# Performance work log

Hardware: AMD Instinct MI355X
Metric: run time of the kernel (lower is better)

Reference implementation:

```python
import jax, jax.numpy as jnp
import numpy as np

NUM_HEADS = 16
HIDDEN = 1024
HEAD = HIDDEN // NUM_HEADS


def setup_inputs() -> dict:
    key = jax.random.key(0)
    k1, k2, k3, k4, k5 = jax.random.split(key, 5)
    b, s, d = 2, 2048, HIDDEN
    scale = 1.0 / np.sqrt(d)
    return {
        "features": jax.random.normal(k1, (b, s, d), dtype=jnp.float32),
        "qkv_w": jax.random.normal(k2, (3 * d, d), dtype=jnp.float32) * scale,  # torch Linear weight [out,in]
        "qkv_b": jax.random.normal(k3, (3 * d,), dtype=jnp.float32) * 0.01,
        "out_w": jax.random.normal(k4, (d, d), dtype=jnp.float32) * scale,
        "out_b": jax.random.normal(k5, (d,), dtype=jnp.float32) * 0.01,
        "use_causal_mask": 0,
    }


def reference(features, qkv_w, qkv_b, out_w, out_b, use_causal_mask):
    b, s, d = features.shape
    qkv = features @ qkv_w.T + qkv_b                      # [b,s,3d]
    q, k, v = jnp.split(qkv, 3, axis=-1)
    # [b,s,d] -> [b,h,s,hd]
    def heads(x):
        return x.reshape(b, s, NUM_HEADS, HEAD).transpose(0, 2, 1, 3)
    q, k, v = heads(q), heads(k), heads(v)
    scores = jnp.einsum("bhqd,bhkd->bhqk", q, k) / np.sqrt(HEAD)
    if use_causal_mask:
        mask = jnp.triu(jnp.ones((s, s), dtype=bool), k=1)
        scores = jnp.where(mask, -jnp.inf, scores)
    attn = jax.nn.softmax(scores, axis=-1)
    out = jnp.einsum("bhqk,bhkd->bhqd", attn, v)          # [b,h,s,hd]
    out = out.transpose(0, 2, 1, 3).reshape(b, s, d)
    return out @ out_w.T + out_b
```

## Files before the change

kernel.cpp:

```cpp
#include <hip/hip_runtime.h>
#include <math.h>

#define BATCH 2
#define SEQ   2048
#define HID   1024
#define NHEAD 16
#define ROWS  (BATCH*SEQ)
#define QKV_N (3*HID)

#define Q_SCALE 0.18033688011112042f

typedef __attribute__((ext_vector_type(8))) short bf16x8;
typedef __attribute__((ext_vector_type(4))) float f32x4;

__device__ __forceinline__ unsigned short f2b(float f) {
    unsigned u = __float_as_uint(f);
    u += 0x7FFF + ((u >> 16) & 1);
    return (unsigned short)(u >> 16);
}
__device__ __forceinline__ unsigned pk2(float a, float b) {
    return (unsigned)f2b(a) | ((unsigned)f2b(b) << 16);
}

#define GLOAD_LDS16(gp, lp) \
    __builtin_amdgcn_global_load_lds((const __attribute__((address_space(1))) void*)(gp), \
                                     (__attribute__((address_space(3))) void*)(lp), 16, 0, 0)

__global__ __launch_bounds__(256)
void cvt_all(const float* __restrict__ a, unsigned short* __restrict__ oa, int na4,
             const float* __restrict__ b, unsigned short* __restrict__ ob, int nb4,
             const float* __restrict__ c, unsigned short* __restrict__ oc, int nc4) {
    int i = blockIdx.x * 256 + threadIdx.x;
    const float* src; unsigned short* dst; int j;
    if (i < na4)            { src = a; dst = oa; j = i; }
    else if (i < na4 + nb4) { src = b; dst = ob; j = i - na4; }
    else if (i < na4 + nb4 + nc4) { src = c; dst = oc; j = i - na4 - nb4; }
    else return;
    float4 v = reinterpret_cast<const float4*>(src)[j];
    ushort4 o;
    o.x = f2b(v.x); o.y = f2b(v.y); o.z = f2b(v.z); o.w = f2b(v.w);
    reinterpret_cast<ushort4*>(dst)[j] = o;
}

template<int MODE>
__global__ __launch_bounds__(256)
void gemm_mfma(const unsigned short* __restrict__ A, const unsigned short* __restrict__ B,
               const float* __restrict__ bias, void* __restrict__ Cout,
               unsigned short* __restrict__ vt, int M, int N, int K) {
    __shared__ __align__(16) unsigned short As[128 * 32];
    __shared__ __align__(16) unsigned short Bs[128 * 32];
    const int tid = threadIdx.x;
    const int w = tid >> 6, l = tid & 63;
    const int wm = w >> 1, wn = w & 1;
    const int l15 = l & 15, l4 = l >> 4;
    const long row0 = (long)blockIdx.y * 128;
    const long col0 = (long)blockIdx.x * 128;

    f32x4 acc[4][4];
    #pragma unroll
    for (int m = 0; m < 4; ++m)
        #pragma unroll
        for (int n = 0; n < 4; ++n) acc[m][n] = (f32x4)0.0f;

    const int lr   = l >> 2;
    const int slot = (l & 3) ^ (lr & 3);

    for (int k0 = 0; k0 < K; k0 += 32) {
        __syncthreads();
        #pragma unroll
        for (int c = 0; c < 2; ++c) {
            int r = w * 32 + c * 16 + lr;
            GLOAD_LDS16(A + (row0 + r) * K + k0 + slot * 8, As + (w * 32 + c * 16) * 32);
            GLOAD_LDS16(B + (col0 + r) * K + k0 + slot * 8, Bs + (w * 32 + c * 16) * 32);
        }
        __syncthreads();

        bf16x8 af[4], bfr[4];
        #pragma unroll
        for (int m = 0; m < 4; ++m) {
            int row = wm * 64 + m * 16 + l15;
            af[m] = *(const bf16x8*)((const char*)As + row * 64 + ((l4 ^ (row & 3)) << 4));
        }
        #pragma unroll
        for (int n = 0; n < 4; ++n) {
            int row = wn * 64 + n * 16 + l15;
            bfr[n] = *(const bf16x8*)((const char*)Bs + row * 64 + ((l4 ^ (row & 3)) << 4));
        }
        #pragma unroll
        for (int m = 0; m < 4; ++m)
            #pragma unroll
            for (int n = 0; n < 4; ++n)
                acc[m][n] = __builtin_amdgcn_mfma_f32_16x16x32_bf16(af[m], bfr[n], acc[m][n], 0, 0, 0);
    }

    #pragma unroll
    for (int m = 0; m < 4; ++m) {
        #pragma unroll
        for (int n = 0; n < 4; ++n) {
            long ccol = col0 + wn * 64 + n * 16 + l15;
            float bv = bias[ccol];
            #pragma unroll
            for (int r2 = 0; r2 < 4; ++r2) {
                long crow = row0 + wm * 64 + m * 16 + l4 * 4 + r2;
                float v = acc[m][n][r2] + bv;
                if (MODE == 0) {
                    ((float*)Cout)[crow * N + ccol] = v;
                } else {
                    if (ccol < 1024) {
                        ((unsigned short*)Cout)[crow * QKV_N + ccol] = f2b(v * Q_SCALE);
                    } else if (ccol < 2048) {
                        ((unsigned short*)Cout)[crow * QKV_N + ccol] = f2b(v);
                    } else {
                        long cc = ccol - 2048;
                        long h = cc >> 6, d = cc & 63;
                        long b = crow >> 11, s = crow & 2047;
                        vt[(((b * NHEAD + h) * 64 + d) << 11) + s] = f2b(v);
                    }
                }
            }
        }
    }
}

__global__ __launch_bounds__(256)
void attn_mfma(const unsigned short* __restrict__ qkv, const unsigned short* __restrict__ vt,
               unsigned short* __restrict__ attno, const int* __restrict__ use_mask) {
    __shared__ __align__(16) unsigned short Ks [64 * 64];
    __shared__ __align__(16) unsigned short Vts[64 * 64];
    __shared__ __align__(16) unsigned short Ps [4][32 * 64];
    const int tid = threadIdx.x;
    const int w = tid >> 6, l = tid & 63;
    const int l15 = l & 15, l4 = l >> 4;
    const int bid  = blockIdx.x;
    const int orig = (bid & 7) * 64 + (bid >> 3);
    const int qt = orig & 15, bh = orig >> 4;
    const int b = bh >> 4, h = bh & 15;
    const int q0 = qt * 128;
    const int wq0 = q0 + w * 32;
    const int causal = use_mask[0];
    const int NT = causal ? 2 * (qt + 1) : (SEQ / 64);

    bf16x8 qf[2][2];
    #pragma unroll
    for (int m = 0; m < 2; ++m) {
        const unsigned short* qp = qkv + (size_t)(b * SEQ + wq0 + m * 16 + l15) * QKV_N + h * 64;
        qf[m][0] = *(const bf16x8*)(qp + l4 * 8);
        qf[m][1] = *(const bf16x8*)(qp + 32 + l4 * 8);
    }

    f32x4 o_acc[2][4];
    #pragma unroll
    for (int m = 0; m < 2; ++m)
        #pragma unroll
        for (int n = 0; n < 4; ++n) o_acc[m][n] = (f32x4)0.0f;
    f32x4 l_acc[2] = {(f32x4)0.0f, (f32x4)0.0f};

    bf16x8 ones;
    #pragma unroll
    for (int j = 0; j < 8; ++j) ones[j] = (short)0x3F80;

    const int srow = l >> 3, g = l & 7;
    const int r0   = w * 16 + srow;
    const int wso  = (g ^ srow) << 3;
    const unsigned short* kbase = qkv + (size_t)b * SEQ * QKV_N + HID + h * 64;
    const unsigned short* vbase = vt + (size_t)bh * 64 * SEQ;
    unsigned short* pw = Ps[w];

    bf16x8 kreg[2], vreg[2];
    #pragma unroll
    for (int c = 0; c < 2; ++c) {
        kreg[c] = *(const bf16x8*)(kbase + (size_t)(r0 + c * 8) * QKV_N + g * 8);
        vreg[c] = *(const bf16x8*)(vbase + (size_t)(r0 + c * 8) * SEQ + g * 8);
    }

    for (int kt = 0; kt < NT; ++kt) {
        __syncthreads();
        #pragma unroll
        for (int c = 0; c < 2; ++c) {
            *(bf16x8*)(Ks  + (r0 + c * 8) * 64 + wso) = kreg[c];
            *(bf16x8*)(Vts + (r0 + c * 8) * 64 + wso) = vreg[c];
        }
        __syncthreads();

        if (kt + 1 < NT) {
            int nk0 = (kt + 1) * 64;
            #pragma unroll
            for (int c = 0; c < 2; ++c) {
                kreg[c] = *(const bf16x8*)(kbase + (size_t)(nk0 + r0 + c * 8) * QKV_N + g * 8);
                vreg[c] = *(const bf16x8*)(vbase + (size_t)(r0 + c * 8) * SEQ + nk0 + g * 8);
            }
        }

        f32x4 s_acc[4][2];
        #pragma unroll
        for (int n = 0; n < 4; ++n)
            #pragma unroll
            for (int m = 0; m < 2; ++m) s_acc[n][m] = (f32x4)0.0f;
        #pragma unroll
        for (int ks = 0; ks < 2; ++ks) {
            #pragma unroll
            for (int n = 0; n < 4; ++n) {
                int row = n * 16 + l15;
                bf16x8 kf = *(const bf16x8*)((const char*)Ks + row * 128 + (((ks * 4 + l4) ^ (row & 7)) << 4));
                #pragma unroll
                for (int m = 0; m < 2; ++m)
                    s_acc[n][m] = __builtin_amdgcn_mfma_f32_16x16x32_bf16(kf, qf[m][ks], s_acc[n][m], 0, 0, 0);
            }
        }
        if (causal) {
            int kk0 = kt * 64;
            #pragma unroll
            for (int n = 0; n < 4; ++n)
                #pragma unroll
                for (int m = 0; m < 2; ++m)
                    #pragma unroll
                    for (int r2 = 0; r2 < 4; ++r2) {
                        int krow = kk0 + n * 16 + l4 * 4 + r2;
                        int qcol = wq0 + m * 16 + l15;
                        if (krow > qcol) s_acc[n][m][r2] = -INFINITY;
                    }
        }

        #pragma unroll
        for (int m = 0; m < 2; ++m) {
            int prow = m * 16 + l15;
            #pragma unroll
            for (int n = 0; n < 4; ++n) {
                float p0 = exp2f(s_acc[n][m][0]);
                float p1 = exp2f(s_acc[n][m][1]);
                float p2 = exp2f(s_acc[n][m][2]);
                float p3 = exp2f(s_acc[n][m][3]);
                uint2 pk;
                pk.x = pk2(p0, p1);
                pk.y = pk2(p2, p3);
                int byteoff = (n * 32 + l4 * 8) ^ ((prow & 7) << 4);
                *(uint2*)((char*)pw + prow * 128 + byteoff) = pk;
            }
        }

        #pragma unroll
        for (int ks = 0; ks < 2; ++ks) {
            bf16x8 pf[2];
            #pragma unroll
            for (int m = 0; m < 2; ++m) {
                int row = m * 16 + l15;
                pf[m] = *(const bf16x8*)((const char*)pw + row * 128 + (((ks * 4 + l4) ^ (row & 7)) << 4));
                l_acc[m] = __builtin_amdgcn_mfma_f32_16x16x32_bf16(pf[m], ones, l_acc[m], 0, 0, 0);
            }
            #pragma unroll
            for (int n = 0; n < 4; ++n) {
                int vrow = n * 16 + l15;
                bf16x8 vf = *(const bf16x8*)((const char*)Vts + vrow * 128 + (((ks * 4 + l4) ^ (vrow & 7)) << 4));
                #pragma unroll
                for (int m = 0; m < 2; ++m)
                    o_acc[m][n] = __builtin_amdgcn_mfma_f32_16x16x32_bf16(pf[m], vf, o_acc[m][n], 0, 0, 0);
            }
        }
    }

    #pragma unroll
    for (int m = 0; m < 2; ++m) {
        #pragma unroll
        for (int r2 = 0; r2 < 4; ++r2) {
            float inv = 1.0f / l_acc[m][r2];
            size_t orow = (size_t)(b * SEQ + wq0 + m * 16 + l4 * 4 + r2);
            #pragma unroll
            for (int n = 0; n < 4; ++n)
                attno[orow * HID + h * 64 + n * 16 + l15] = f2b(o_acc[m][n][r2] * inv);
        }
    }
}

extern "C" void kernel_launch(void* const* d_in, const int* in_sizes, int n_in,
                              void* d_out, int out_size, void* d_ws, size_t ws_size,
                              hipStream_t stream) {
    const float* features = (const float*)d_in[0];
    const float* qkv_w    = (const float*)d_in[1];
    const float* qkv_b    = (const float*)d_in[2];
    const float* out_w    = (const float*)d_in[3];
    const float* out_b    = (const float*)d_in[4];
    const int*   use_mask = (const int*)d_in[5];

    char* ws = (char*)d_ws;
    unsigned short* fbf     = (unsigned short*)(ws);
    unsigned short* wbf     = (unsigned short*)(ws + 8388608);
    unsigned short* owbf    = (unsigned short*)(ws + 14680064);
    unsigned short* qkvbf   = (unsigned short*)(ws + 16777216);
    unsigned short* vtbuf   = (unsigned short*)(ws + 41943040);
    unsigned short* attnobf = (unsigned short*)(ws + 50331648);

    cvt_all<<<8192, 256, 0, stream>>>(features, fbf, 1048576,
                                      qkv_w, wbf, 786432,
                                      out_w, owbf, 262144);

    dim3 g1(QKV_N / 128, ROWS / 128);
    gemm_mfma<2><<<g1, 256, 0, stream>>>(fbf, wbf, qkv_b, (void*)qkvbf, vtbuf,
                                         ROWS, QKV_N, HID);

    attn_mfma<<<512, 256, 0, stream>>>(qkvbf, vtbuf, attnobf, use_mask);

    dim3 g3(HID / 128, ROWS / 128);
    gemm_mfma<0><<<g3, 256, 0, stream>>>(attnobf, owbf, out_b, d_out, (unsigned short*)nullptr,
                                         ROWS, HID, HID);
}
```

Measured before the change: 156.0 us.

## Split attention key tiles across wave pairs and double grid size

The attention kernel now uses 64-query blocks with 1024 blocks instead of 128-query blocks with 512. Each pair of waves shares a 32-query slice but handles a different 32-key half of every key tile. The partial output and row sums of the two halves are combined through LDS at the end. It also adds s_setprio around the MFMA sections, a packed bf16 conversion intrinsic, occupancy launch bounds and incremental pointer arithmetic. The aim is more parallelism and occupancy on the device, at the cost of loading K/V tiles twice as often per query and an extra reduction step.

```diff
diff --git a/kernel.cpp b/kernel.cpp
--- a/kernel.cpp
+++ b/kernel.cpp
@@ -1,4 +1,5 @@
 #include <hip/hip_runtime.h>
+#include <hip/hip_bf16.h>
 #include <math.h>
 
 #define BATCH 2
@@ -18,8 +19,10 @@
     u += 0x7FFF + ((u >> 16) & 1);
     return (unsigned short)(u >> 16);
 }
-__device__ __forceinline__ unsigned pk2(float a, float b) {
-    return (unsigned)f2b(a) | ((unsigned)f2b(b) << 16);
+__device__ __forceinline__ unsigned pk2c(float a, float b) {
+    __hip_bfloat162 h = __float22bfloat162_rn(float2{a, b});
+    union { __hip_bfloat162 h2; unsigned u; } cv; cv.h2 = h;
+    return cv.u;
 }
 
 #define GLOAD_LDS16(gp, lp) \
@@ -122,23 +125,24 @@
     }
 }
 
-__global__ __launch_bounds__(256)
+__global__ __launch_bounds__(256, 4)
 void attn_mfma(const unsigned short* __restrict__ qkv, const unsigned short* __restrict__ vt,
                unsigned short* __restrict__ attno, const int* __restrict__ use_mask) {
     __shared__ __align__(16) unsigned short Ks [64 * 64];
     __shared__ __align__(16) unsigned short Vts[64 * 64];
-    __shared__ __align__(16) unsigned short Ps [4][32 * 64];
+    __shared__ __align__(16) unsigned short Ps [4][32 * 32];
     const int tid = threadIdx.x;
     const int w = tid >> 6, l = tid & 63;
     const int l15 = l & 15, l4 = l >> 4;
     const int bid  = blockIdx.x;
-    const int orig = (bid & 7) * 64 + (bid >> 3);
-    const int qt = orig & 15, bh = orig >> 4;
+    const int orig = (bid & 7) * 128 + (bid >> 3);
+    const int qt = orig & 31, bh = orig >> 5;
     const int b = bh >> 4, h = bh & 15;
-    const int q0 = qt * 128;
-    const int wq0 = q0 + w * 32;
+    const int q0 = qt * 64;
+    const int qh = w & 1, kh = w >> 1;
+    const int wq0 = q0 + qh * 32;
     const int causal = use_mask[0];
-    const int NT = causal ? 2 * (qt + 1) : (SEQ / 64);
+    const int NT = causal ? (qt + 1) : (SEQ / 64);
 
     bf16x8 qf[2][2];
     #pragma unroll
@@ -162,16 +166,19 @@
     const int srow = l >> 3, g = l & 7;
     const int r0   = w * 16 + srow;
     const int wso  = (g ^ srow) << 3;
-    const unsigned short* kbase = qkv + (size_t)b * SEQ * QKV_N + HID + h * 64;
-    const unsigned short* vbase = vt + (size_t)bh * 64 * SEQ;
     unsigned short* pw = Ps[w];
 
+    const unsigned short* kp = qkv + (size_t)b * SEQ * QKV_N + HID + h * 64
+                                   + (size_t)r0 * QKV_N + g * 8;
+    const unsigned short* vp = vt + (size_t)bh * 64 * SEQ + (size_t)r0 * SEQ + g * 8;
+
     bf16x8 kreg[2], vreg[2];
-    #pragma unroll
-    for (int c = 0; c < 2; ++c) {
-        kreg[c] = *(const bf16x8*)(kbase + (size_t)(r0 + c * 8) * QKV_N + g * 8);
-        vreg[c] = *(const bf16x8*)(vbase + (size_t)(r0 + c * 8) * SEQ + g * 8);
-    }
+    kreg[0] = *(const bf16x8*)(kp);
+    kreg[1] = *(const bf16x8*)(kp + 8 * QKV_N);
+    vreg[0] = *(const bf16x8*)(vp);
+    vreg[1] = *(const bf16x8*)(vp + 8 * SEQ);
+    kp += (size_t)64 * QKV_N;
+    vp += 64;
 
     for (int kt = 0; kt < NT; ++kt) {
         __syncthreads();
@@ -183,41 +190,44 @@
         __syncthreads();
 
         if (kt + 1 < NT) {
-            int nk0 = (kt + 1) * 64;
-            #pragma unroll
-            for (int c = 0; c < 2; ++c) {
-                kreg[c] = *(const bf16x8*)(kbase + (size_t)(nk0 + r0 + c * 8) * QKV_N + g * 8);
-                vreg[c] = *(const bf16x8*)(vbase + (size_t)(r0 + c * 8) * SEQ + nk0 + g * 8);
-            }
-        }
-
-        f32x4 s_acc[4][2];
-        #pragma unroll
-        for (int n = 0; n < 4; ++n)
-            #pragma unroll
-            for (int m = 0; m < 2; ++m) s_acc[n][m] = (f32x4)0.0f;
+            kreg[0] = *(const bf16x8*)(kp);
+            kreg[1] = *(const bf16x8*)(kp + 8 * QKV_N);
+            vreg[0] = *(const bf16x8*)(vp);
+            vreg[1] = *(const bf16x8*)(vp + 8 * SEQ);
+            kp += (size_t)64 * QKV_N;
+            vp += 64;
+        }
+
+        f32x4 s_acc[2][2];
+        #pragma unroll
+        for (int n2 = 0; n2 < 2; ++n2)
+            #pragma unroll
+            for (int m = 0; m < 2; ++m) s_acc[n2][m] = (f32x4)0.0f;
+        __builtin_amdgcn_s_setprio(1);
         #pragma unroll
         for (int ks = 0; ks < 2; ++ks) {
             #pragma unroll
-            for (int n = 0; n < 4; ++n) {
-                int row = n * 16 + l15;
+            for (int n2 = 0; n2 < 2; ++n2) {
+                int row = kh * 32 + n2 * 16 + l15;
                 bf16x8 kf = *(const bf16x8*)((const char*)Ks + row * 128 + (((ks * 4 + l4) ^ (row & 7)) << 4));
                 #pragma unroll
                 for (int m = 0; m < 2; ++m)
-                    s_acc[n][m] = __builtin_amdgcn_mfma_f32_16x16x32_bf16(kf, qf[m][ks], s_acc[n][m], 0, 0, 0);
-            }
-        }
+                    s_acc[n2][m] = __builtin_amdgcn_mfma_f32_16x16x32_bf16(kf, qf[m][ks], s_acc[n2][m], 0, 0, 0);
+            }
+        }
+        __builtin_amdgcn_s_setprio(0);
+
         if (causal) {
-            int kk0 = kt * 64;
-            #pragma unroll
-            for (int n = 0; n < 4; ++n)
+            int kk0 = kt * 64 + kh * 32;
+            #pragma unroll
+            for (int n2 = 0; n2 < 2; ++n2)
                 #pragma unroll
                 for (int m = 0; m < 2; ++m)
                     #pragma unroll
                     for (int r2 = 0; r2 < 4; ++r2) {
-                        int krow = kk0 + n * 16 + l4 * 4 + r2;
+                        int krow = kk0 + n2 * 16 + l4 * 4 + r2;
                         int qcol = wq0 + m * 16 + l15;
-                        if (krow > qcol) s_acc[n][m][r2] = -INFINITY;
+                        if (krow > qcol) s_acc[n2][m][r2] = -INFINITY;
                     }
         }
 
@@ -225,48 +235,70 @@
         for (int m = 0; m < 2; ++m) {
             int prow = m * 16 + l15;
             #pragma unroll
-            for (int n = 0; n < 4; ++n) {
-                float p0 = exp2f(s_acc[n][m][0]);
-                float p1 = exp2f(s_acc[n][m][1]);
-                float p2 = exp2f(s_acc[n][m][2]);
-                float p3 = exp2f(s_acc[n][m][3]);
+            for (int n2 = 0; n2 < 2; ++n2) {
+                float p0 = exp2f(s_acc[n2][m][0]);
+                float p1 = exp2f(s_acc[n2][m][1]);
+                float p2 = exp2f(s_acc[n2][m][2]);
+                float p3 = exp2f(s_acc[n2][m][3]);
                 uint2 pk;
-                pk.x = pk2(p0, p1);
-                pk.y = pk2(p2, p3);
-                int byteoff = (n * 32 + l4 * 8) ^ ((prow & 7) << 4);
-                *(uint2*)((char*)pw + prow * 128 + byteoff) = pk;
-            }
-        }
-
-        #pragma unroll
-        for (int ks = 0; ks < 2; ++ks) {
-            bf16x8 pf[2];
-            #pragma unroll
-            for (int m = 0; m < 2; ++m) {
-                int row = m * 16 + l15;
-                pf[m] = *(const bf16x8*)((const char*)pw + row * 128 + (((ks * 4 + l4) ^ (row & 7)) << 4));
-                l_acc[m] = __builtin_amdgcn_mfma_f32_16x16x32_bf16(pf[m], ones, l_acc[m], 0, 0, 0);
-            }
-            #pragma unroll
-            for (int n = 0; n < 4; ++n) {
-                int vrow = n * 16 + l15;
-                bf16x8 vf = *(const bf16x8*)((const char*)Vts + vrow * 128 + (((ks * 4 + l4) ^ (vrow & 7)) << 4));
+                pk.x = pk2c(p0, p1);
+                pk.y = pk2c(p2, p3);
+                int byteoff = (n2 * 32 + l4 * 8) ^ ((prow & 3) << 4);
+                *(uint2*)((char*)pw + prow * 64 + byteoff) = pk;
+            }
+        }
+
+        __builtin_amdgcn_s_setprio(1);
+        bf16x8 pf[2];
+        #pragma unroll
+        for (int m = 0; m < 2; ++m) {
+            int prow = m * 16 + l15;
+            pf[m] = *(const bf16x8*)((const char*)pw + prow * 64 + ((l4 * 16) ^ ((prow & 3) << 4)));
+            l_acc[m] = __builtin_amdgcn_mfma_f32_16x16x32_bf16(pf[m], ones, l_acc[m], 0, 0, 0);
+        }
+        #pragma unroll
+        for (int n = 0; n < 4; ++n) {
+            int vrow = n * 16 + l15;
+            bf16x8 vf = *(const bf16x8*)((const char*)Vts + vrow * 128 + (((kh * 4 + l4) ^ (vrow & 7)) << 4));
+            #pragma unroll
+            for (int m = 0; m < 2; ++m)
+                o_acc[m][n] = __builtin_amdgcn_mfma_f32_16x16x32_bf16(pf[m], vf, o_acc[m][n], 0, 0, 0);
+        }
+        __builtin_amdgcn_s_setprio(0);
+    }
+
+    __syncthreads();
+    float* mq = (float*)(qh ? Vts : Ks);
+    float* lb = (float*)&Ps[0][0];
+    if (kh == 1) {
+        #pragma unroll
+        for (int m = 0; m < 2; ++m) {
+            #pragma unroll
+            for (int r2 = 0; r2 < 4; ++r2) {
+                int qr = m * 16 + l4 * 4 + r2;
                 #pragma unroll
-                for (int m = 0; m < 2; ++m)
-                    o_acc[m][n] = __builtin_amdgcn_mfma_f32_16x16x32_bf16(pf[m], vf, o_acc[m][n], 0, 0, 0);
-            }
-        }
-    }
-
-    #pragma unroll
-    for (int m = 0; m < 2; ++m) {
-        #pragma unroll
-        for (int r2 = 0; r2 < 4; ++r2) {
-            float inv = 1.0f / l_acc[m][r2];
-            size_t orow = (size_t)(b * SEQ + wq0 + m * 16 + l4 * 4 + r2);
-            #pragma unroll
-            for (int n = 0; n < 4; ++n)
-                attno[orow * HID + h * 64 + n * 16 + l15] = f2b(o_acc[m][n][r2] * inv);
+                for (int n = 0; n < 4; ++n)
+                    mq[qr * 64 + n * 16 + l15] = o_acc[m][n][r2];
+                if (l15 == 0) lb[qh * 32 + qr] = l_acc[m][r2];
+            }
+        }
+    }
+    __syncthreads();
+    if (kh == 0) {
+        #pragma unroll
+        for (int m = 0; m < 2; ++m) {
+            #pragma unroll
+            for (int r2 = 0; r2 < 4; ++r2) {
+                int qr = m * 16 + l4 * 4 + r2;
+                float lt = l_acc[m][r2] + lb[qh * 32 + qr];
+                float inv = 1.0f / lt;
+                size_t orow = (size_t)(b * SEQ + wq0 + qr);
+                #pragma unroll
+                for (int n = 0; n < 4; ++n) {
+                    float o = o_acc[m][n][r2] + mq[qr * 64 + n * 16 + l15];
+                    attno[orow * HID + h * 64 + n * 16 + l15] = f2b(o * inv);
+                }
+            }
         }
     }
 }
@@ -297,7 +329,7 @@
     gemm_mfma<2><<<g1, 256, 0, stream>>>(fbf, wbf, qkv_b, (void*)qkvbf, vtbuf,
                                          ROWS, QKV_N, HID);
 
-    attn_mfma<<<512, 256, 0, stream>>>(qkvbf, vtbuf, attnobf, use_mask);
+    attn_mfma<<<1024, 256, 0, stream>>>(qkvbf, vtbuf, attnobf, use_mask);
 
     dim3 g3(HID / 128, ROWS / 128);
     gemm_mfma<0><<<g3, 256, 0, stream>>>(attnobf, owbf, out_b, d_out, (unsigned short*)nullptr,
```

Result: faster. 148.4 us (-4.9%).
